# Kernel optimization log

Hardware: AMD Instinct MI355X
Metric: run time of the kernel (lower is better)

Reference implementation:

```python
import jax, jax.numpy as jnp
import numpy as np

B, S, H = 2, 2048, 2048
NUM_HEADS, HEAD_DIM, GROUP_SIZE = 16, 128, 4
NUM_KV_HEADS = NUM_HEADS // GROUP_SIZE
ROPE_THETA = 10000.0


def setup_inputs() -> dict:
    key = jax.random.key(0)
    ks = jax.random.split(key, 10)
    xavier = lambda k, fi, fo: jax.random.uniform(k, (fi, fo), jnp.float32,
                                                  -jnp.sqrt(6.0 / (fi + fo)), jnp.sqrt(6.0 / (fi + fo)))
    hidden_states = jax.random.normal(ks[0], (B, S, H), jnp.float32)
    # causal mask: 1.0 where attention is disallowed (strictly upper triangle)
    mask = jnp.triu(jnp.ones((S, S), jnp.float32), k=1)[None, None, :, :]
    mask = jnp.broadcast_to(mask, (B, 1, S, S))
    return {
        "hidden_states": hidden_states,
        "mask": mask,
        "Wq": xavier(ks[1], H, NUM_HEADS * HEAD_DIM), "bq": jnp.zeros((NUM_HEADS * HEAD_DIM,), jnp.float32),
        "Wk": xavier(ks[2], H, NUM_KV_HEADS * HEAD_DIM), "bk": jnp.zeros((NUM_KV_HEADS * HEAD_DIM,), jnp.float32),
        "Wv": xavier(ks[3], H, NUM_KV_HEADS * HEAD_DIM), "bv": jnp.zeros((NUM_KV_HEADS * HEAD_DIM,), jnp.float32),
        "Wo": xavier(ks[4], NUM_HEADS * HEAD_DIM, H), "bo": jnp.zeros((H,), jnp.float32),
    }


def _apply_rope(q, k):
    # q: [b, s, hq, d], k: [b, s, hk, d]
    s, d = q.shape[1], q.shape[-1]
    inv_freq = 1.0 / (ROPE_THETA ** (jnp.arange(0, d, 2, dtype=jnp.float32) / d))  # [d/2]
    angles = jnp.arange(s, dtype=jnp.float32)[:, None] * inv_freq[None, :]          # [s, d/2]
    cos = jnp.cos(angles)[None, :, None, :]  # [1, s, 1, d/2]
    sin = jnp.sin(angles)[None, :, None, :]

    def rot(x):
        x1, x2 = jnp.split(x, 2, axis=-1)
        return jnp.concatenate([x1 * cos - x2 * sin, x1 * sin + x2 * cos], axis=-1)

    return rot(q), rot(k)


def reference(hidden_states, mask, Wq, bq, Wk, bk, Wv, bv, Wo, bo):
    b, s, _ = hidden_states.shape
    scale = 1.0 / jnp.sqrt(jnp.float32(HEAD_DIM))

    q = (hidden_states @ Wq + bq).reshape(b, s, NUM_HEADS, HEAD_DIM)
    k = (hidden_states @ Wk + bk).reshape(b, s, NUM_KV_HEADS, HEAD_DIM)
    v = (hidden_states @ Wv + bv).reshape(b, s, NUM_KV_HEADS, HEAD_DIM)

    q, k = _apply_rope(q, k)

    q = jnp.transpose(q, (0, 2, 1, 3))  # [b, hq, s, d]
    k = jnp.transpose(k, (0, 2, 1, 3))  # [b, hk, s, d]
    v = jnp.transpose(v, (0, 2, 1, 3))

    new_past_key, new_past_value = k, v

    # GQA: repeat each KV head group_size times
    k_rep = jnp.repeat(k, GROUP_SIZE, axis=1)  # [b, hq, s, d]
    v_rep = jnp.repeat(v, GROUP_SIZE, axis=1)

    attn_scores = jnp.einsum('bhqd,bhkd->bhqk', q, k_rep) * scale  # [b, hq, s, s]
    attn_scores = attn_scores + mask * -1e9
    attn_probs = jax.nn.softmax(attn_scores, axis=-1)
    attn_output = jnp.einsum('bhqk,bhkd->bhqd', attn_probs, v_rep)

    attn_output = attn_output.transpose(0, 2, 1, 3).reshape(b, s, NUM_HEADS * HEAD_DIM)
    attn_output = attn_output @ Wo + bo
    return attn_output, new_past_key, new_past_value
```

## Files before the change

kernel.cpp:

```cpp
#include <hip/hip_runtime.h>
#include <stdint.h>

#define S_LEN 2048
#define HDIM  2048
#define N_HEADS 16
#define HEAD_D 128
#define N_KV 4

typedef unsigned short u16;
typedef __attribute__((ext_vector_type(8))) short bf16x8;
typedef __attribute__((ext_vector_type(4))) float f32x4;

__device__ __forceinline__ u16 f2bf(float f) {
  unsigned u = __float_as_uint(f);
  u += 0x7FFFu + ((u >> 16) & 1u);
  return (u16)(u >> 16);
}

__device__ __forceinline__ void gll16(void* lds, const void* gp) {
  __builtin_amdgcn_global_load_lds(
      (const __attribute__((address_space(1))) void*)gp,
      (__attribute__((address_space(3))) void*)lds, 16, 0, 0);
}

__global__ __launch_bounds__(256) void k_convert(const float* __restrict__ src,
                                                 u16* __restrict__ dst, int n4) {
  int i = blockIdx.x * 256 + threadIdx.x;
  if (i < n4) {
    float4 v = ((const float4*)src)[i];
    ushort4 o;
    o.x = f2bf(v.x); o.y = f2bf(v.y); o.z = f2bf(v.z); o.w = f2bf(v.w);
    ((ushort4*)dst)[i] = o;
  }
}

__global__ __launch_bounds__(256) void k_transpose_w(const float* __restrict__ W,
                                                     u16* __restrict__ Wt,
                                                     int K, int N) {
  __shared__ float tile[64][65];
  int k0 = blockIdx.x * 64, n0 = blockIdx.y * 64;
  int tr = threadIdx.x >> 6, tc = threadIdx.x & 63;
#pragma unroll
  for (int i = 0; i < 16; ++i) {
    int r = tr + i * 4;
    tile[r][tc] = W[(size_t)(k0 + r) * N + n0 + tc];
  }
  __syncthreads();
#pragma unroll
  for (int i = 0; i < 16; ++i) {
    int r = tr + i * 4;
    Wt[(size_t)(n0 + r) * K + k0 + tc] = f2bf(tile[tc][r]);
  }
}

__device__ __forceinline__ void gemm_tile_128(
    const u16* __restrict__ A, const u16* __restrict__ Bt,
    const float* __restrict__ bias, float* __restrict__ C,
    int m0, int n0, int K, int ldc) {
  __shared__ __align__(16) u16 sA[128 * 32];
  __shared__ __align__(16) u16 sB[128 * 32];
  const int tid = threadIdx.x;
  const int lane = tid & 63;
  const int wave = tid >> 6;
  const int quad = lane >> 4;
  const int l15 = lane & 15;
  const int wm = (wave >> 1) << 6;
  const int wn = (wave & 1) << 6;

  f32x4 acc[4][4];
#pragma unroll
  for (int i = 0; i < 4; ++i)
#pragma unroll
    for (int j = 0; j < 4; ++j)
      acc[i][j] = (f32x4){0.f, 0.f, 0.f, 0.f};

  for (int kk = 0; kk < K; kk += 32) {
    __syncthreads();
#pragma unroll
    for (int it = 0; it < 2; ++it) {
      int c = tid + (it << 8);
      int row = c >> 2;
      int ko = (c & 3) << 3;
      gll16((char*)sA + c * 16, A + (size_t)(m0 + row) * K + kk + ko);
      gll16((char*)sB + c * 16, Bt + (size_t)(n0 + row) * K + kk + ko);
    }
    __syncthreads();
    bf16x8 af[4], bfr[4];
#pragma unroll
    for (int i = 0; i < 4; ++i)
      af[i] = *(const bf16x8*)&sA[(wm + (i << 4) + l15) * 32 + quad * 8];
#pragma unroll
    for (int j = 0; j < 4; ++j)
      bfr[j] = *(const bf16x8*)&sB[(wn + (j << 4) + l15) * 32 + quad * 8];
#pragma unroll
    for (int i = 0; i < 4; ++i)
#pragma unroll
      for (int j = 0; j < 4; ++j)
        acc[i][j] = __builtin_amdgcn_mfma_f32_16x16x32_bf16(af[i], bfr[j], acc[i][j], 0, 0, 0);
  }

#pragma unroll
  for (int i = 0; i < 4; ++i) {
    int row = m0 + wm + (i << 4) + quad * 4;
#pragma unroll
    for (int j = 0; j < 4; ++j) {
      int col = n0 + wn + (j << 4) + l15;
      float bv = bias[col];
      float* cp = C + (size_t)row * ldc + col;
#pragma unroll
      for (int r = 0; r < 4; ++r)
        cp[(size_t)r * ldc] = acc[i][j][r] + bv;
    }
  }
}

__global__ __launch_bounds__(256) void k_gemm_qkv(
    const u16* __restrict__ X, const u16* __restrict__ Wqt,
    const u16* __restrict__ Wkt, const u16* __restrict__ Wvt,
    const float* __restrict__ bq, const float* __restrict__ bk,
    const float* __restrict__ bv, float* __restrict__ Qf,
    float* __restrict__ Kf, float* __restrict__ Vf) {
  int m0 = blockIdx.x << 7;
  int by = blockIdx.y;
  const u16* Bt; const float* bias; float* C; int n0, ldc;
  if (by < 16)      { Bt = Wqt; bias = bq; C = Qf; n0 = by << 7;        ldc = 2048; }
  else if (by < 20) { Bt = Wkt; bias = bk; C = Kf; n0 = (by - 16) << 7; ldc = 512;  }
  else              { Bt = Wvt; bias = bv; C = Vf; n0 = (by - 20) << 7; ldc = 512;  }
  gemm_tile_128(X, Bt, bias, C, m0, n0, 2048, ldc);
}

__global__ __launch_bounds__(256) void k_gemm_o(
    const u16* __restrict__ A, const u16* __restrict__ Wot,
    const float* __restrict__ bo, float* __restrict__ C) {
  gemm_tile_128(A, Wot, bo, C, blockIdx.x << 7, blockIdx.y << 7, 2048, 2048);
}

__global__ __launch_bounds__(256) void k_rope(
    const float* __restrict__ Qf, const float* __restrict__ Kf,
    u16* __restrict__ Qbf, u16* __restrict__ Kbf, float* __restrict__ outK) {
  const int bx = blockIdx.x;
  const int b = bx >> 11;
  const int s = bx & 2047;
  const int tid = threadIdx.x;
  const float qscale = 0.08838834764831845f;
  const float c1 = -13.287712379549449f / 64.f;

#pragma unroll
  for (int it = 0; it < 4; ++it) {
    int p = tid + (it << 8);
    int hh = p >> 6;
    int ii = p & 63;
    float ang = (float)s * exp2f((float)ii * c1);
    float cs, sn;
    sincosf(ang, &sn, &cs);
    const float* src = Qf + (size_t)bx * 2048 + hh * 128 + ii;
    float x1 = src[0], x2 = src[64];
    float o1 = (x1 * cs - x2 * sn) * qscale;
    float o2 = (x1 * sn + x2 * cs) * qscale;
    u16* dst = Qbf + ((size_t)(b * N_HEADS + hh) * S_LEN + s) * HEAD_D + ii;
    dst[0] = f2bf(o1);
    dst[64] = f2bf(o2);
  }
  {
    int hh = tid >> 6;
    int ii = tid & 63;
    float ang = (float)s * exp2f((float)ii * c1);
    float cs, sn;
    sincosf(ang, &sn, &cs);
    const float* src = Kf + (size_t)bx * 512 + hh * 128 + ii;
    float x1 = src[0], x2 = src[64];
    float o1 = x1 * cs - x2 * sn;
    float o2 = x1 * sn + x2 * cs;
    size_t idx = ((size_t)(b * N_KV + hh) * S_LEN + s) * HEAD_D + ii;
    Kbf[idx] = f2bf(o1);
    Kbf[idx + 64] = f2bf(o2);
    outK[idx] = o1;
    outK[idx + 64] = o2;
  }
}

__global__ __launch_bounds__(256) void k_vtrans(const float* __restrict__ Vf,
                                                u16* __restrict__ Vt,
                                                float* __restrict__ outV) {
  __shared__ float tile[64][65];
  int s0 = blockIdx.x * 64, d0 = blockIdx.y * 64;
  int z = blockIdx.z;
  int b = z >> 2, kvh = z & 3;
  int tr = threadIdx.x >> 6, tc = threadIdx.x & 63;
#pragma unroll
  for (int i = 0; i < 16; ++i) {
    int r = tr + i * 4;
    float v = Vf[(size_t)(b * S_LEN + s0 + r) * 512 + kvh * 128 + d0 + tc];
    tile[r][tc] = v;
    outV[((size_t)z * S_LEN + s0 + r) * HEAD_D + d0 + tc] = v;
  }
  __syncthreads();
#pragma unroll
  for (int i = 0; i < 16; ++i) {
    int r = tr + i * 4;
    Vt[((size_t)z * HEAD_D + d0 + r) * S_LEN + s0 + tc] = f2bf(tile[tc][r]);
  }
}

__global__ __launch_bounds__(256, 3) void k_attn(
    const u16* __restrict__ Qbf, const u16* __restrict__ Kbf,
    const u16* __restrict__ Vt, u16* __restrict__ attn) {
  __shared__ __align__(16) u16 smem[22528];
  u16* sK = smem;
  u16* sV = smem + 8704;
  u16* sP = smem + 17920;

  const int tid = threadIdx.x;
  const int lane = tid & 63;
  const int wave = tid >> 6;
  const int quad = lane >> 4;
  const int l15 = lane & 15;

  const int qt = 31 - blockIdx.y;
  const int bh = blockIdx.x;
  const int b = bh >> 4;
  const int h = bh & 15;
  const int kvh = h >> 2;
  const int q0 = qt << 6;

  const u16* Qb = Qbf + ((size_t)(b * N_HEADS + h) * S_LEN + q0) * HEAD_D;
  const u16* Kb = Kbf + (size_t)(b * N_KV + kvh) * S_LEN * HEAD_D;
  const u16* Vb = Vt + (size_t)(b * N_KV + kvh) * HEAD_D * S_LEN;

  bf16x8 aq[4];
#pragma unroll
  for (int kc = 0; kc < 4; ++kc)
    aq[kc] = *(const bf16x8*)(Qb + (size_t)(wave * 16 + l15) * HEAD_D + kc * 32 + quad * 8);

  float mst[4], lst[4];
  f32x4 oacc[8];
#pragma unroll
  for (int r = 0; r < 4; ++r) { mst[r] = -1e30f; lst[r] = 0.f; }
#pragma unroll
  for (int n = 0; n < 8; ++n) oacc[n] = (f32x4){0.f, 0.f, 0.f, 0.f};

  const int ntiles = qt + 1;
  for (int t = 0; t < ntiles; ++t) {
    const int kt0 = t << 6;
    __syncthreads();
#pragma unroll
    for (int it = 0; it < 9; ++it) {
      int c = tid + (it << 8);
      if (c < 1088) {
        int row = c / 17;
        int k16 = c - row * 17;
        gll16((char*)sK + c * 16, Kb + (size_t)(kt0 + row) * HEAD_D + k16 * 8);
      } else if (c < 2240) {
        int vv = c - 1088;
        int d = vv / 9;
        int s16 = vv - d * 9;
        gll16((char*)sV + vv * 16, Vb + (size_t)d * S_LEN + kt0 + s16 * 8);
      }
    }
    __syncthreads();

    f32x4 sc[4];
#pragma unroll
    for (int j = 0; j < 4; ++j) sc[j] = (f32x4){0.f, 0.f, 0.f, 0.f};
#pragma unroll
    for (int kc = 0; kc < 4; ++kc) {
#pragma unroll
      for (int j = 0; j < 4; ++j) {
        bf16x8 bk = *(const bf16x8*)&sK[(j * 16 + l15) * 136 + kc * 32 + quad * 8];
        sc[j] = __builtin_amdgcn_mfma_f32_16x16x32_bf16(aq[kc], bk, sc[j], 0, 0, 0);
      }
    }

    if (t == qt) {
      int qrow = q0 + wave * 16 + quad * 4;
#pragma unroll
      for (int j = 0; j < 4; ++j) {
        int col = kt0 + j * 16 + l15;
#pragma unroll
        for (int r = 0; r < 4; ++r)
          if (col > qrow + r) sc[j][r] = -1e9f;
      }
    }

    float al[4];
#pragma unroll
    for (int r = 0; r < 4; ++r) {
      float m = fmaxf(fmaxf(sc[0][r], sc[1][r]), fmaxf(sc[2][r], sc[3][r]));
#pragma unroll
      for (int off = 1; off < 16; off <<= 1)
        m = fmaxf(m, __shfl_xor(m, off, 64));
      float mn = fmaxf(mst[r], m);
      al[r] = __expf(mst[r] - mn);
      mst[r] = mn;
    }
    float rs[4] = {0.f, 0.f, 0.f, 0.f};
#pragma unroll
    for (int j = 0; j < 4; ++j)
#pragma unroll
      for (int r = 0; r < 4; ++r) {
        float p = __expf(sc[j][r] - mst[r]);
        rs[r] += p;
        sP[(wave * 16 + quad * 4 + r) * 72 + j * 16 + l15] = f2bf(p);
      }
#pragma unroll
    for (int r = 0; r < 4; ++r) {
      float s = rs[r];
#pragma unroll
      for (int off = 1; off < 16; off <<= 1)
        s += __shfl_xor(s, off, 64);
      lst[r] = lst[r] * al[r] + s;
#pragma unroll
      for (int n = 0; n < 8; ++n)
        oacc[n][r] *= al[r];
    }

#pragma unroll
    for (int kc = 0; kc < 2; ++kc) {
      bf16x8 ap = *(const bf16x8*)&sP[(wave * 16 + l15) * 72 + kc * 32 + quad * 8];
#pragma unroll
      for (int n = 0; n < 8; ++n) {
        bf16x8 bv = *(const bf16x8*)&sV[(n * 16 + l15) * 72 + kc * 32 + quad * 8];
        oacc[n] = __builtin_amdgcn_mfma_f32_16x16x32_bf16(ap, bv, oacc[n], 0, 0, 0);
      }
    }
  }

#pragma unroll
  for (int r = 0; r < 4; ++r) {
    int row = q0 + wave * 16 + quad * 4 + r;
    float inv = 1.0f / lst[r];
    u16* op = attn + ((size_t)b * S_LEN + row) * HDIM + h * HEAD_D;
#pragma unroll
    for (int n = 0; n < 8; ++n)
      op[n * 16 + l15] = f2bf(oacc[n][r] * inv);
  }
}

extern "C" void kernel_launch(void* const* d_in, const int* in_sizes, int n_in,
                              void* d_out, int out_size, void* d_ws, size_t ws_size,
                              hipStream_t stream) {
  (void)in_sizes; (void)n_in; (void)out_size; (void)ws_size;
  const float* hs = (const float*)d_in[0];
  const float* Wq = (const float*)d_in[2];
  const float* bq = (const float*)d_in[3];
  const float* Wk = (const float*)d_in[4];
  const float* bk = (const float*)d_in[5];
  const float* Wv = (const float*)d_in[6];
  const float* bv = (const float*)d_in[7];
  const float* Wo = (const float*)d_in[8];
  const float* bo = (const float*)d_in[9];
  float* out = (float*)d_out;

  char* ws = (char*)d_ws;
  u16* Xbf   = (u16*)(ws + 0);
  u16* Wqt   = (u16*)(ws + 16777216);
  u16* Wkt   = (u16*)(ws + 25165824);
  u16* Wvt   = (u16*)(ws + 27262976);
  u16* Wot   = (u16*)(ws + 29360128);
  float* Qf  = (float*)(ws + 37748736);
  float* Kf  = (float*)(ws + 71303168);
  float* Vf  = (float*)(ws + 79691776);
  u16* Qbf   = (u16*)(ws + 88080384);
  u16* Kbf   = (u16*)(ws + 104857600);
  u16* Vtb   = (u16*)(ws + 109051904);
  u16* attnb = (u16*)(ws + 37748736);

  k_convert<<<8192, 256, 0, stream>>>(hs, Xbf, 2097152);
  k_transpose_w<<<dim3(32, 32), 256, 0, stream>>>(Wq, Wqt, 2048, 2048);
  k_transpose_w<<<dim3(32, 8), 256, 0, stream>>>(Wk, Wkt, 2048, 512);
  k_transpose_w<<<dim3(32, 8), 256, 0, stream>>>(Wv, Wvt, 2048, 512);
  k_transpose_w<<<dim3(32, 32), 256, 0, stream>>>(Wo, Wot, 2048, 2048);
  k_gemm_qkv<<<dim3(32, 24), 256, 0, stream>>>(Xbf, Wqt, Wkt, Wvt, bq, bk, bv, Qf, Kf, Vf);
  k_rope<<<4096, 256, 0, stream>>>(Qf, Kf, Qbf, Kbf, out + 8388608);
  k_vtrans<<<dim3(32, 2, 8), 256, 0, stream>>>(Vf, Vtb, out + 10485760);
  k_attn<<<dim3(32, 32), 256, 0, stream>>>(Qbf, Kbf, Vtb, attnb);
  k_gemm_o<<<dim3(32, 16), 256, 0, stream>>>(attnb, Wot, bo, out);
}
```

Baseline: 381.4 us.

## Restructure attention: 128-row query tiles, register-resident P, transposed S MFMA

Doubles the query tile per block to 128 rows (32 per wave), so each K/V tile loaded to LDS is reused by twice as many queries and the grid halves. Scores are computed transposed (K as the A operand), so the probabilities can feed the PV MFMA straight from registers via 16x16x16 instructions, removing the LDS round-trip for P. Softmax switches to exp2 with log2(e) folded into the Q scale in the rope kernel. It adds register pressure from the doubled accumulators, lowers block count, and waves skip fully masked tiles while still joining the loads.

After: 513.8 us. 34.7% more time.

```diff
diff --git a/kernel.cpp b/kernel.cpp
--- a/kernel.cpp
+++ b/kernel.cpp
@@ -9,7 +9,10 @@
 
 typedef unsigned short u16;
 typedef __attribute__((ext_vector_type(8))) short bf16x8;
+typedef __attribute__((ext_vector_type(4))) short bf16x4;
 typedef __attribute__((ext_vector_type(4))) float f32x4;
+
+#define MFMA_PV(a, b, c) __builtin_amdgcn_mfma_f32_16x16x16bf16_1k(a, b, c, 0, 0, 0)
 
 __device__ __forceinline__ u16 f2bf(float f) {
   unsigned u = __float_as_uint(f);
@@ -142,7 +145,7 @@
   const int b = bx >> 11;
   const int s = bx & 2047;
   const int tid = threadIdx.x;
-  const float qscale = 0.08838834764831845f;
+  const float qscale = 0.08838834764831845f * 1.4426950408889634f;
   const float c1 = -13.287712379549449f / 64.f;
 
 #pragma unroll
@@ -205,10 +208,9 @@
 __global__ __launch_bounds__(256, 3) void k_attn(
     const u16* __restrict__ Qbf, const u16* __restrict__ Kbf,
     const u16* __restrict__ Vt, u16* __restrict__ attn) {
-  __shared__ __align__(16) u16 smem[22528];
+  __shared__ __align__(16) u16 smem[17920];
   u16* sK = smem;
   u16* sV = smem + 8704;
-  u16* sP = smem + 17920;
 
   const int tid = threadIdx.x;
   const int lane = tid & 63;
@@ -216,30 +218,33 @@
   const int quad = lane >> 4;
   const int l15 = lane & 15;
 
-  const int qt = 31 - blockIdx.y;
+  const int qt = 15 - blockIdx.y;
   const int bh = blockIdx.x;
   const int b = bh >> 4;
   const int h = bh & 15;
   const int kvh = h >> 2;
-  const int q0 = qt << 6;
-
-  const u16* Qb = Qbf + ((size_t)(b * N_HEADS + h) * S_LEN + q0) * HEAD_D;
+  const int q0 = qt << 7;
+  const int qw = q0 + wave * 32;
+
+  const u16* Qb = Qbf + ((size_t)(b * N_HEADS + h) * S_LEN + qw) * HEAD_D;
   const u16* Kb = Kbf + (size_t)(b * N_KV + kvh) * S_LEN * HEAD_D;
   const u16* Vb = Vt + (size_t)(b * N_KV + kvh) * HEAD_D * S_LEN;
 
-  bf16x8 aq[4];
-#pragma unroll
-  for (int kc = 0; kc < 4; ++kc)
-    aq[kc] = *(const bf16x8*)(Qb + (size_t)(wave * 16 + l15) * HEAD_D + kc * 32 + quad * 8);
-
-  float mst[4], lst[4];
-  f32x4 oacc[8];
-#pragma unroll
-  for (int r = 0; r < 4; ++r) { mst[r] = -1e30f; lst[r] = 0.f; }
-#pragma unroll
-  for (int n = 0; n < 8; ++n) oacc[n] = (f32x4){0.f, 0.f, 0.f, 0.f};
-
-  const int ntiles = qt + 1;
+  bf16x8 aq[2][4];
+#pragma unroll
+  for (int i = 0; i < 2; ++i)
+#pragma unroll
+    for (int kc = 0; kc < 4; ++kc)
+      aq[i][kc] = *(const bf16x8*)(Qb + (size_t)(i * 16 + l15) * HEAD_D + kc * 32 + quad * 8);
+
+  float mst[2] = {-1e30f, -1e30f}, lst[2] = {0.f, 0.f};
+  f32x4 oacc[2][8];
+#pragma unroll
+  for (int i = 0; i < 2; ++i)
+#pragma unroll
+    for (int n = 0; n < 8; ++n) oacc[i][n] = (f32x4){0.f, 0.f, 0.f, 0.f};
+
+  const int ntiles = 2 * qt + 2;
   for (int t = 0; t < ntiles; ++t) {
     const int kt0 = t << 6;
     __syncthreads();
@@ -259,81 +264,96 @@
     }
     __syncthreads();
 
-    f32x4 sc[4];
-#pragma unroll
-    for (int j = 0; j < 4; ++j) sc[j] = (f32x4){0.f, 0.f, 0.f, 0.f};
+    if (kt0 > qw + 31) continue;
+
+    f32x4 st[2][4];
+#pragma unroll
+    for (int i = 0; i < 2; ++i)
+#pragma unroll
+      for (int j = 0; j < 4; ++j) st[i][j] = (f32x4){0.f, 0.f, 0.f, 0.f};
 #pragma unroll
     for (int kc = 0; kc < 4; ++kc) {
 #pragma unroll
       for (int j = 0; j < 4; ++j) {
-        bf16x8 bk = *(const bf16x8*)&sK[(j * 16 + l15) * 136 + kc * 32 + quad * 8];
-        sc[j] = __builtin_amdgcn_mfma_f32_16x16x32_bf16(aq[kc], bk, sc[j], 0, 0, 0);
-      }
-    }
-
-    if (t == qt) {
-      int qrow = q0 + wave * 16 + quad * 4;
+        bf16x8 kf = *(const bf16x8*)&sK[(j * 16 + l15) * 136 + kc * 32 + quad * 8];
+#pragma unroll
+        for (int i = 0; i < 2; ++i)
+          st[i][j] = __builtin_amdgcn_mfma_f32_16x16x32_bf16(kf, aq[i][kc], st[i][j], 0, 0, 0);
+      }
+    }
+
+    if (kt0 + 63 > qw) {
+#pragma unroll
+      for (int i = 0; i < 2; ++i) {
+        int q = qw + i * 16 + l15;
+#pragma unroll
+        for (int j = 0; j < 4; ++j) {
+          int s = kt0 + j * 16 + quad * 4;
+#pragma unroll
+          for (int r = 0; r < 4; ++r)
+            if (s + r > q) st[i][j][r] = -1e9f;
+        }
+      }
+    }
+
+    bf16x4 pf[2][4];
+    float al[2];
+#pragma unroll
+    for (int i = 0; i < 2; ++i) {
+      float m = -1e30f;
+#pragma unroll
+      for (int j = 0; j < 4; ++j)
+#pragma unroll
+        for (int r = 0; r < 4; ++r) m = fmaxf(m, st[i][j][r]);
+      m = fmaxf(m, __shfl_xor(m, 16, 64));
+      m = fmaxf(m, __shfl_xor(m, 32, 64));
+      float mn = fmaxf(mst[i], m);
+      al[i] = exp2f(mst[i] - mn);
+      mst[i] = mn;
+      float rs = 0.f;
 #pragma unroll
       for (int j = 0; j < 4; ++j) {
-        int col = kt0 + j * 16 + l15;
-#pragma unroll
-        for (int r = 0; r < 4; ++r)
-          if (col > qrow + r) sc[j][r] = -1e9f;
-      }
-    }
-
-    float al[4];
+#pragma unroll
+        for (int r = 0; r < 4; ++r) {
+          float p = exp2f(st[i][j][r] - mn);
+          rs += p;
+          pf[i][j][r] = (short)f2bf(p);
+        }
+      }
+      rs += __shfl_xor(rs, 16, 64);
+      rs += __shfl_xor(rs, 32, 64);
+      lst[i] = lst[i] * al[i] + rs;
+#pragma unroll
+      for (int r = 0; r < 4; ++r) {
+        float a = __shfl(al[i], quad * 4 + r, 16);
+#pragma unroll
+        for (int n = 0; n < 8; ++n) oacc[i][n][r] *= a;
+      }
+    }
+
+#pragma unroll
+    for (int j = 0; j < 4; ++j) {
+#pragma unroll
+      for (int n = 0; n < 8; ++n) {
+        bf16x4 vf = *(const bf16x4*)&sV[(n * 16 + l15) * 72 + j * 16 + quad * 4];
+#pragma unroll
+        for (int i = 0; i < 2; ++i)
+          oacc[i][n] = MFMA_PV(pf[i][j], vf, oacc[i][n]);
+      }
+    }
+  }
+
+#pragma unroll
+  for (int i = 0; i < 2; ++i)
 #pragma unroll
     for (int r = 0; r < 4; ++r) {
-      float m = fmaxf(fmaxf(sc[0][r], sc[1][r]), fmaxf(sc[2][r], sc[3][r]));
-#pragma unroll
-      for (int off = 1; off < 16; off <<= 1)
-        m = fmaxf(m, __shfl_xor(m, off, 64));
-      float mn = fmaxf(mst[r], m);
-      al[r] = __expf(mst[r] - mn);
-      mst[r] = mn;
-    }
-    float rs[4] = {0.f, 0.f, 0.f, 0.f};
-#pragma unroll
-    for (int j = 0; j < 4; ++j)
-#pragma unroll
-      for (int r = 0; r < 4; ++r) {
-        float p = __expf(sc[j][r] - mst[r]);
-        rs[r] += p;
-        sP[(wave * 16 + quad * 4 + r) * 72 + j * 16 + l15] = f2bf(p);
-      }
-#pragma unroll
-    for (int r = 0; r < 4; ++r) {
-      float s = rs[r];
-#pragma unroll
-      for (int off = 1; off < 16; off <<= 1)
-        s += __shfl_xor(s, off, 64);
-      lst[r] = lst[r] * al[r] + s;
+      float inv = 1.0f / __shfl(lst[i], quad * 4 + r, 16);
+      int row = qw + i * 16 + quad * 4 + r;
+      u16* op = attn + ((size_t)b * S_LEN + row) * HDIM + h * HEAD_D;
 #pragma unroll
       for (int n = 0; n < 8; ++n)
-        oacc[n][r] *= al[r];
-    }
-
-#pragma unroll
-    for (int kc = 0; kc < 2; ++kc) {
-      bf16x8 ap = *(const bf16x8*)&sP[(wave * 16 + l15) * 72 + kc * 32 + quad * 8];
-#pragma unroll
-      for (int n = 0; n < 8; ++n) {
-        bf16x8 bv = *(const bf16x8*)&sV[(n * 16 + l15) * 72 + kc * 32 + quad * 8];
-        oacc[n] = __builtin_amdgcn_mfma_f32_16x16x32_bf16(ap, bv, oacc[n], 0, 0, 0);
-      }
-    }
-  }
-
-#pragma unroll
-  for (int r = 0; r < 4; ++r) {
-    int row = q0 + wave * 16 + quad * 4 + r;
-    float inv = 1.0f / lst[r];
-    u16* op = attn + ((size_t)b * S_LEN + row) * HDIM + h * HEAD_D;
-#pragma unroll
-    for (int n = 0; n < 8; ++n)
-      op[n * 16 + l15] = f2bf(oacc[n][r] * inv);
-  }
+        op[n * 16 + l15] = f2bf(oacc[i][n][r] * inv);
+    }
 }
 
 extern "C" void kernel_launch(void* const* d_in, const int* in_sizes, int n_in,
@@ -373,6 +393,6 @@
   k_gemm_qkv<<<dim3(32, 24), 256, 0, stream>>>(Xbf, Wqt, Wkt, Wvt, bq, bk, bv, Qf, Kf, Vf);
   k_rope<<<4096, 256, 0, stream>>>(Qf, Kf, Qbf, Kbf, out + 8388608);
   k_vtrans<<<dim3(32, 2, 8), 256, 0, stream>>>(Vf, Vtb, out + 10485760);
-  k_attn<<<dim3(32, 32), 256, 0, stream>>>(Qbf, Kbf, Vtb, attnb);
+  k_attn<<<dim3(32, 16), 256, 0, stream>>>(Qbf, Kbf, Vtb, attnb);
   k_gemm_o<<<dim3(32, 16), 256, 0, stream>>>(attnb, Wot, bo, out);
 }
```
